# Kernel optimization log

Hardware: AMD Instinct MI355X
Metric: run time of the kernel (lower is better)

The kernel has to match this reference:

```python
import jax, jax.numpy as jnp
import numpy as np


def setup_inputs() -> dict:
    key = jax.random.key(0)
    k1, k2 = jax.random.split(key)
    B, N, M, D = 8, 8192, 8192, 3
    x = jax.random.normal(k1, (B, N, D), dtype=jnp.float32)
    y = jax.random.normal(k2, (B, M, D), dtype=jnp.float32)
    return {"x": x, "y": y}


def reference(x, y):
    # dist[b, i, j] = |x_bi|^2 + |y_bj|^2 - 2 * <x_bi, y_bj>
    # (same math as the torch code's rx.transpose(2,1) + ry - 2*xy, but
    #  computed with row-norm vectors instead of full NxN / MxM bmms)
    xx = jnp.sum(x * x, axis=-1)                      # [B, N]
    yy = jnp.sum(y * y, axis=-1)                      # [B, M]
    xy = jnp.einsum('bnd,bmd->bnm', x, y)             # [B, N, M]
    dist = xx[:, :, None] + yy[:, None, :] - 2.0 * xy # [B, N, M]
    dist1 = jnp.min(dist, axis=1)  # min over x points -> per-y nearest  [B, M]
    dist2 = jnp.min(dist, axis=2)  # min over y points -> per-x nearest  [B, N]
    return jnp.mean(dist1) + jnp.mean(dist2)
```

## Files before the change

kernel.cpp:

```cpp
#include <hip/hip_runtime.h>


#define B_ 8
#define N_ 8192
#define PTS (B_ * N_)
#define TPB 512

typedef short bf16x8 __attribute__((ext_vector_type(8)));
typedef float f32x16 __attribute__((ext_vector_type(16)));

__device__ __forceinline__ unsigned b16(float f) {
  unsigned u = __float_as_uint(f);
  return (u + 0x7FFFu + ((u >> 16) & 1u)) >> 16;
}
__device__ __forceinline__ float bf(unsigned h) { return __uint_as_float(h << 16); }

__global__ __launch_bounds__(TPB) void chamfer_k(
    const float* __restrict__ x, const float* __restrict__ y,
    float* __restrict__ out) {
  __shared__ uint4 ldsFrag[32 * 64];
  __shared__ float red[8];

  const unsigned one = 0x3F80u;
  int t = threadIdx.x, lane = t & 63, w = t >> 6;
  int b = blockIdx.x;
  int dir = b >> 8;
  int bb = b & 255;
  int batch = bb >> 5;
  int rowSeg = bb & 31;
  const float* __restrict__ own  = dir ? y : x;
  const float* __restrict__ cand = dir ? x : y;

  int m = lane & 31;
  int row0 = batch * N_ + rowSeg * 256 + w * 32;
  const float* po = own + 3 * (row0 + m);
  float v0 = po[0], v1 = po[1], v2 = po[2];
  float nv = fmaf(v0, v0, fmaf(v1, v1, v2 * v2));
  float a0 = -2.0f * v0, a1 = -2.0f * v1, a2 = -2.0f * v2;
  unsigned ah0 = b16(a0), ah1 = b16(a1), ah2 = b16(a2);
  unsigned al0 = b16(a0 - bf(ah0)), al1 = b16(a1 - bf(ah1)), al2 = b16(a2 - bf(ah2));
  unsigned nh = b16(nv), nl = b16(nv - bf(nh));
  uint4 h0 = make_uint4(ah0 | (ah1 << 16), ah2 | (ah0 << 16),
                        ah1 | (ah2 << 16), al0 | (al1 << 16));
  uint4 h1 = make_uint4(al2 | (nh << 16), nl | (one << 16), one, 0u);
  uint4 afr;
  afr.x = (lane < 32) ? h0.x : h1.x;
  afr.y = (lane < 32) ? h0.y : h1.y;
  afr.z = (lane < 32) ? h0.z : h1.z;
  afr.w = (lane < 32) ? h0.w : h1.w;
  bf16x8 A = __builtin_bit_cast(bf16x8, afr);

  f32x16 z = {0.f,0.f,0.f,0.f,0.f,0.f,0.f,0.f,0.f,0.f,0.f,0.f,0.f,0.f,0.f,0.f};
  f32x16 rm;
#pragma unroll
  for (int r = 0; r < 16; ++r) rm[r] = 1e30f;

  const float* cbb = cand + batch * N_ * 3;
  for (int ch = 0; ch < 8; ++ch) {
    __syncthreads();
    const float* cb = cbb + ch * 1024 * 3;
#pragma unroll
    for (int q = 0; q < 2; ++q) {
      int p = 2 * t + q;
      float c0 = cb[3 * p], c1 = cb[3 * p + 1], c2 = cb[3 * p + 2];
      float nc = fmaf(c0, c0, fmaf(c1, c1, c2 * c2));
      unsigned yh0 = b16(c0), yh1 = b16(c1), yh2 = b16(c2);
      unsigned yl0 = b16(c0 - bf(yh0)), yl1 = b16(c1 - bf(yh1)), yl2 = b16(c2 - bf(yh2));
      unsigned ch_ = b16(nc), cl_ = b16(nc - bf(ch_));
      int tt = p >> 5, mm = p & 31;
      ldsFrag[tt * 64 + mm]      = make_uint4(yh0 | (yh1 << 16), yh2 | (yl0 << 16),
                                              yl1 | (yl2 << 16), yh0 | (yh1 << 16));
      ldsFrag[tt * 64 + 32 + mm] = make_uint4(yh2 | (one << 16), one | (ch_ << 16),
                                              cl_, 0u);
    }
    __syncthreads();

#pragma unroll 4
    for (int i = 0; i < 16; ++i) {
      bf16x8 B0 = __builtin_bit_cast(bf16x8, ldsFrag[(2 * i) * 64 + lane]);
      bf16x8 B1 = __builtin_bit_cast(bf16x8, ldsFrag[(2 * i + 1) * 64 + lane]);
      f32x16 acc0 = __builtin_amdgcn_mfma_f32_32x32x16_bf16(A, B0, z, 0, 0, 0);
      f32x16 acc1 = __builtin_amdgcn_mfma_f32_32x32x16_bf16(A, B1, z, 0, 0, 0);
#pragma unroll
      for (int r = 0; r < 16; ++r)
        rm[r] = fminf(fminf(rm[r], acc0[r]), acc1[r]);
    }
  }

#pragma unroll
  for (int msk = 1; msk <= 16; msk <<= 1) {
#pragma unroll
    for (int r = 0; r < 16; ++r)
      rm[r] = fminf(rm[r], __shfl_xor(rm[r], msk, 64));
  }
  float s = 0.0f;
#pragma unroll
  for (int r = 0; r < 16; ++r) s += rm[r];
  s += __shfl_xor(s, 32, 64);
  if (lane == 0) red[w] = s;
  __syncthreads();
  if (t == 0) {
    float bs = 0.0f;
#pragma unroll
    for (int c = 0; c < 8; ++c) bs += red[c];
    atomicAdd(out, bs * (1.0f / (float)PTS));
  }
}

extern "C" void kernel_launch(void* const* d_in, const int* in_sizes, int n_in,
                              void* d_out, int out_size, void* d_ws, size_t ws_size,
                              hipStream_t stream) {
  const float* x = (const float*)d_in[0];
  const float* y = (const float*)d_in[1];
  float* out = (float*)d_out;
  hipMemsetAsync(out, 0, sizeof(float), stream);
  chamfer_k<<<512, TPB, 0, stream>>>(x, y, out);
}
```

Before: 97.09 us.

## Double-buffer candidate LDS fragments and split min accumulators

```diff
diff --git a/kernel.cpp b/kernel.cpp
--- a/kernel.cpp
+++ b/kernel.cpp
@@ -15,10 +15,29 @@
 }
 __device__ __forceinline__ float bf(unsigned h) { return __uint_as_float(h << 16); }
 
-__global__ __launch_bounds__(TPB) void chamfer_k(
+__device__ __forceinline__ void build_chunk(const float* __restrict__ cb,
+                                            uint4* __restrict__ dst, int t) {
+  const unsigned one = 0x3F80u;
+#pragma unroll
+  for (int q = 0; q < 2; ++q) {
+    int p = t + q * TPB;
+    float c0 = cb[3 * p], c1 = cb[3 * p + 1], c2 = cb[3 * p + 2];
+    float nc = fmaf(c0, c0, fmaf(c1, c1, c2 * c2));
+    unsigned yh0 = b16(c0), yh1 = b16(c1), yh2 = b16(c2);
+    unsigned yl0 = b16(c0 - bf(yh0)), yl1 = b16(c1 - bf(yh1)), yl2 = b16(c2 - bf(yh2));
+    unsigned nh = b16(nc), nl = b16(nc - bf(nh));
+    int tt = p >> 5, mm = p & 31;
+    dst[tt * 64 + mm]      = make_uint4(yh0 | (yh1 << 16), yh2 | (yl0 << 16),
+                                        yl1 | (yl2 << 16), yh0 | (yh1 << 16));
+    dst[tt * 64 + 32 + mm] = make_uint4(yh2 | (one << 16), one | (nh << 16),
+                                        nl, 0u);
+  }
+}
+
+__global__ __launch_bounds__(TPB, 4) void chamfer_k(
     const float* __restrict__ x, const float* __restrict__ y,
     float* __restrict__ out) {
-  __shared__ uint4 ldsFrag[32 * 64];
+  __shared__ uint4 ldsFrag[2][32 * 64];
   __shared__ float red[8];
 
   const unsigned one = 0x3F80u;
@@ -51,51 +70,49 @@
   bf16x8 A = __builtin_bit_cast(bf16x8, afr);
 
   f32x16 z = {0.f,0.f,0.f,0.f,0.f,0.f,0.f,0.f,0.f,0.f,0.f,0.f,0.f,0.f,0.f,0.f};
-  f32x16 rm;
+  f32x16 rmA, rmB;
 #pragma unroll
-  for (int r = 0; r < 16; ++r) rm[r] = 1e30f;
+  for (int r = 0; r < 16; ++r) { rmA[r] = 1e30f; rmB[r] = 1e30f; }
 
   const float* cbb = cand + batch * N_ * 3;
+  build_chunk(cbb, ldsFrag[0], t);
+  __syncthreads();
+
   for (int ch = 0; ch < 8; ++ch) {
-    __syncthreads();
-    const float* cb = cbb + ch * 1024 * 3;
+    const uint4* cur = ldsFrag[ch & 1];
+    if (ch < 7)
+      build_chunk(cbb + (ch + 1) * 1024 * 3, ldsFrag[(ch + 1) & 1], t);
+
+#pragma unroll 2
+    for (int i = 0; i < 8; ++i) {
+      bf16x8 B0 = __builtin_bit_cast(bf16x8, cur[(4 * i + 0) * 64 + lane]);
+      bf16x8 B1 = __builtin_bit_cast(bf16x8, cur[(4 * i + 1) * 64 + lane]);
+      bf16x8 B2 = __builtin_bit_cast(bf16x8, cur[(4 * i + 2) * 64 + lane]);
+      bf16x8 B3 = __builtin_bit_cast(bf16x8, cur[(4 * i + 3) * 64 + lane]);
+      f32x16 acc0 = __builtin_amdgcn_mfma_f32_32x32x16_bf16(A, B0, z, 0, 0, 0);
+      f32x16 acc1 = __builtin_amdgcn_mfma_f32_32x32x16_bf16(A, B1, z, 0, 0, 0);
+      f32x16 acc2 = __builtin_amdgcn_mfma_f32_32x32x16_bf16(A, B2, z, 0, 0, 0);
+      f32x16 acc3 = __builtin_amdgcn_mfma_f32_32x32x16_bf16(A, B3, z, 0, 0, 0);
 #pragma unroll
-    for (int q = 0; q < 2; ++q) {
-      int p = 2 * t + q;
-      float c0 = cb[3 * p], c1 = cb[3 * p + 1], c2 = cb[3 * p + 2];
-      float nc = fmaf(c0, c0, fmaf(c1, c1, c2 * c2));
-      unsigned yh0 = b16(c0), yh1 = b16(c1), yh2 = b16(c2);
-      unsigned yl0 = b16(c0 - bf(yh0)), yl1 = b16(c1 - bf(yh1)), yl2 = b16(c2 - bf(yh2));
-      unsigned ch_ = b16(nc), cl_ = b16(nc - bf(ch_));
-      int tt = p >> 5, mm = p & 31;
-      ldsFrag[tt * 64 + mm]      = make_uint4(yh0 | (yh1 << 16), yh2 | (yl0 << 16),
-                                              yl1 | (yl2 << 16), yh0 | (yh1 << 16));
-      ldsFrag[tt * 64 + 32 + mm] = make_uint4(yh2 | (one << 16), one | (ch_ << 16),
-                                              cl_, 0u);
+      for (int r = 0; r < 16; ++r) {
+        rmA[r] = fminf(fminf(rmA[r], acc0[r]), acc1[r]);
+        rmB[r] = fminf(fminf(rmB[r], acc2[r]), acc3[r]);
+      }
     }
     __syncthreads();
-
-#pragma unroll 4
-    for (int i = 0; i < 16; ++i) {
-      bf16x8 B0 = __builtin_bit_cast(bf16x8, ldsFrag[(2 * i) * 64 + lane]);
-      bf16x8 B1 = __builtin_bit_cast(bf16x8, ldsFrag[(2 * i + 1) * 64 + lane]);
-      f32x16 acc0 = __builtin_amdgcn_mfma_f32_32x32x16_bf16(A, B0, z, 0, 0, 0);
-      f32x16 acc1 = __builtin_amdgcn_mfma_f32_32x32x16_bf16(A, B1, z, 0, 0, 0);
-#pragma unroll
-      for (int r = 0; r < 16; ++r)
-        rm[r] = fminf(fminf(rm[r], acc0[r]), acc1[r]);
-    }
   }
 
+#pragma unroll
+  for (int r = 0; r < 16; ++r) rmA[r] = fminf(rmA[r], rmB[r]);
 #pragma unroll
   for (int msk = 1; msk <= 16; msk <<= 1) {
 #pragma unroll
     for (int r = 0; r < 16; ++r)
-      rm[r] = fminf(rm[r], __shfl_xor(rm[r], msk, 64));
+      rmA[r] = fminf(rmA[r], __shfl_xor(rmA[r], msk, 64));
   }
   float s = 0.0f;
 #pragma unroll
-  for (int r = 0; r < 16; ++r) s += rm[r];
+  for (int r = 0; r < 16; ++r) s += rmA[r];
   s += __shfl_xor(s, 32, 64);
   if (lane == 0) red[w] = s;
   __syncthreads();
```

After: 95.56 us. No clear change (-1.6%).
